# Performance work log

Measured on AMD Instinct MI355X. Metric: run time of the kernel, lower is better.

Reference implementation:

```python
import jax, jax.numpy as jnp
import numpy as np
import math

L, B, S, D, H, DI, V = 4, 2, 1024, 768, 12, 3072, 512
DK = D // H

def gelu_tanh(x):
    c = math.sqrt(2.0 / math.pi)
    return 0.5 * x * (1.0 + jnp.tanh(c * (x + 0.044715 * x ** 3)))

def layer_norm(x, g, b, eps=1e-5):
    mu = jnp.mean(x, axis=-1, keepdims=True)
    var = jnp.var(x, axis=-1, keepdims=True)
    return (x - mu) * jax.lax.rsqrt(var + eps) * g + b

def setup_inputs() -> dict:
    key = jax.random.key(0)
    ks = jax.random.split(key, 12)
    w = 0.02  # init scale
    return {
        "x": jax.random.randint(ks[0], (B, S), 0, V),
        "embed": jax.random.normal(ks[1], (V, D), jnp.float32) * w,
        "pos_emb": jax.random.normal(ks[2], (S, D), jnp.float32) * w,
        "ln1_g": jnp.ones((L, D), jnp.float32),
        "ln1_b": jnp.zeros((L, D), jnp.float32),
        "wq": jax.random.normal(ks[3], (L, D, D), jnp.float32) * w,
        "bq": jnp.zeros((L, D), jnp.float32),
        "wk": jax.random.normal(ks[4], (L, D, D), jnp.float32) * w,
        "bk": jnp.zeros((L, D), jnp.float32),
        "wv": jax.random.normal(ks[5], (L, D, D), jnp.float32) * w,
        "bv": jnp.zeros((L, D), jnp.float32),
        "wo": jax.random.normal(ks[6], (L, D, D), jnp.float32) * w,
        "bo": jnp.zeros((L, D), jnp.float32),
        "ln2_g": jnp.ones((L, D), jnp.float32),
        "ln2_b": jnp.zeros((L, D), jnp.float32),
        "w_in": jax.random.normal(ks[7], (L, D, DI), jnp.float32) * w,
        "b_in": jnp.zeros((L, DI), jnp.float32),
        "w_out": jax.random.normal(ks[8], (L, DI, D), jnp.float32) * w,
        "b_out": jnp.zeros((L, D), jnp.float32),
        "lnf_g": jnp.ones((D,), jnp.float32),
        "lnf_b": jnp.zeros((D,), jnp.float32),
        "out_w": jax.random.normal(ks[9], (D, V), jnp.float32) * w,
    }

def reference(x, embed, pos_emb, ln1_g, ln1_b, wq, bq, wk, bk, wv, bv, wo, bo,
              ln2_g, ln2_b, w_in, b_in, w_out, b_out, lnf_g, lnf_b, out_w):
    s = x.shape[1]
    h = embed[x] + pos_emb[None, :s]                       # [B,S,D]
    causal = jnp.tril(jnp.ones((s, s), bool))              # True = keep
    scale = 1.0 / math.sqrt(DK)
    for l in range(L):
        a = layer_norm(h, ln1_g[l], ln1_b[l])
        q = (a @ wq[l] + bq[l]).reshape(-1, s, H, DK)
        k = (a @ wk[l] + bk[l]).reshape(-1, s, H, DK)
        v = (a @ wv[l] + bv[l]).reshape(-1, s, H, DK)
        scores = jnp.einsum('bqhd,bkhd->bhqk', q, k) * scale
        scores = jnp.where(causal, scores, -jnp.inf)
        attn = jax.nn.softmax(scores, axis=-1)
        o = jnp.einsum('bhqk,bkhd->bqhd', attn, v).reshape(-1, s, D)
        h = h + o @ wo[l] + bo[l]
        f = layer_norm(h, ln2_g[l], ln2_b[l])
        h = h + gelu_tanh(f @ w_in[l] + b_in[l]) @ w_out[l] + b_out[l]
    h = layer_norm(h, lnf_g, lnf_b)
    return h @ out_w                                       # [B,S,V] logits
```

## Files before the change

kernel.cpp:

```cpp
#include <hip/hip_runtime.h>
#include <hip/hip_bf16.h>


#define TKN    2048
#define DMODEL 768
#define SEQ    1024
#define NH     12
#define DHEAD  64
#define DFF    3072
#define NL     4
#define NVOCAB 512
#define NQKV   2304

typedef unsigned short u16;
typedef __attribute__((ext_vector_type(4))) float f32x4;
typedef __attribute__((ext_vector_type(8))) short short8;
typedef __attribute__((ext_vector_type(4))) unsigned short us4;

__device__ __forceinline__ u16 f2bf(float f) {
  unsigned u = __builtin_bit_cast(unsigned, f);
  u += 0x7fffu + ((u >> 16) & 1u);
  return (u16)(u >> 16);
}

__device__ __forceinline__ short8 mk8(us4 lo, us4 hi) {
  short8 r;
  r[0] = (short)lo[0]; r[1] = (short)lo[1]; r[2] = (short)lo[2]; r[3] = (short)lo[3];
  r[4] = (short)hi[0]; r[5] = (short)hi[1]; r[6] = (short)hi[2]; r[7] = (short)hi[3];
  return r;
}

__device__ __forceinline__ void gload16(const u16* g, u16* l) {
  __builtin_amdgcn_global_load_lds(
      (const __attribute__((address_space(1))) unsigned int*)g,
      (__attribute__((address_space(3))) unsigned int*)l, 16, 0, 0);
}

__global__ __launch_bounds__(256) void k_embed(const int* __restrict__ x,
                                               const float* __restrict__ emb,
                                               const float* __restrict__ pos,
                                               float* __restrict__ h) {
  int t = blockIdx.x;
  int s = t & (SEQ - 1);
  int id = x[t];
  int d = threadIdx.x;
#pragma unroll
  for (int j = 0; j < 3; ++j, d += 256)
    h[t * DMODEL + d] = emb[id * DMODEL + d] + pos[s * DMODEL + d];
}

__global__ __launch_bounds__(256) void k_ln(const float* __restrict__ h,
                                            const float* __restrict__ gam,
                                            const float* __restrict__ bet,
                                            u16* __restrict__ out) {
  __shared__ float sbuf[8];
  int row = blockIdx.x, tid = threadIdx.x;
  const float* hr = h + (size_t)row * DMODEL;
  float x0 = hr[tid], x1 = hr[tid + 256], x2 = hr[tid + 512];
  float s = x0 + x1 + x2;
#pragma unroll
  for (int off = 32; off > 0; off >>= 1) s += __shfl_down(s, off);
  if ((tid & 63) == 0) sbuf[tid >> 6] = s;
  __syncthreads();
  float mu = (sbuf[0] + sbuf[1] + sbuf[2] + sbuf[3]) * (1.0f / DMODEL);
  float d0 = x0 - mu, d1 = x1 - mu, d2 = x2 - mu;
  float v = d0 * d0 + d1 * d1 + d2 * d2;
#pragma unroll
  for (int off = 32; off > 0; off >>= 1) v += __shfl_down(v, off);
  if ((tid & 63) == 0) sbuf[4 + (tid >> 6)] = v;
  __syncthreads();
  float var = (sbuf[4] + sbuf[5] + sbuf[6] + sbuf[7]) * (1.0f / DMODEL);
  float rstd = rsqrtf(var + 1e-5f);
  size_t o = (size_t)row * DMODEL;
  out[o + tid]       = f2bf(d0 * rstd * gam[tid]       + bet[tid]);
  out[o + tid + 256] = f2bf(d1 * rstd * gam[tid + 256] + bet[tid + 256]);
  out[o + tid + 512] = f2bf(d2 * rstd * gam[tid + 512] + bet[tid + 512]);
}

__device__ __forceinline__ void cvt_tile(const float* __restrict__ src, int ldS,
                                         int k0, int n0src,
                                         u16* __restrict__ dst, int ldD, int n0dst,
                                         int tid, u16 (*tl)[72]) {
  int kr = tid >> 2, nj = (tid & 3) << 4;
  const float* sp = src + (size_t)(k0 + kr) * ldS + n0src + nj;
  float4 a0 = ((const float4*)sp)[0];
  float4 a1 = ((const float4*)sp)[1];
  float4 a2 = ((const float4*)sp)[2];
  float4 a3 = ((const float4*)sp)[3];
  u16* tr = &tl[kr][nj];
  tr[0]=f2bf(a0.x); tr[1]=f2bf(a0.y); tr[2]=f2bf(a0.z); tr[3]=f2bf(a0.w);
  tr[4]=f2bf(a1.x); tr[5]=f2bf(a1.y); tr[6]=f2bf(a1.z); tr[7]=f2bf(a1.w);
  tr[8]=f2bf(a2.x); tr[9]=f2bf(a2.y); tr[10]=f2bf(a2.z); tr[11]=f2bf(a2.w);
  tr[12]=f2bf(a3.x); tr[13]=f2bf(a3.y); tr[14]=f2bf(a3.z); tr[15]=f2bf(a3.w);
  __syncthreads();
  int nr = tid >> 2, kj = (tid & 3) << 4;
  us4 o[4];
#pragma unroll
  for (int c = 0; c < 4; ++c)
#pragma unroll
    for (int i = 0; i < 4; ++i) o[c][i] = tl[kj + c * 4 + i][nr];
  u16* dp = dst + (size_t)(n0dst + nr) * ldD + k0 + kj;
  ((us4*)dp)[0] = o[0]; ((us4*)dp)[1] = o[1];
  ((us4*)dp)[2] = o[2]; ((us4*)dp)[3] = o[3];
}

__global__ __launch_bounds__(256) void k_cvtL(const float* __restrict__ wq,
                                              const float* __restrict__ wk,
                                              const float* __restrict__ wv,
                                              const float* __restrict__ wo,
                                              const float* __restrict__ win,
                                              const float* __restrict__ wout,
                                              u16* __restrict__ wqkvT,
                                              u16* __restrict__ woT,
                                              u16* __restrict__ winT,
                                              u16* __restrict__ woutT) {
  __shared__ u16 tl[64][72];
  int t = blockIdx.x, tid = threadIdx.x;
  if (t < 432) {
    int kt = t % 12, ntile = t / 12;
    int gn0 = ntile * 64, sel = gn0 / DMODEL;
    const float* src = sel == 0 ? wq : sel == 1 ? wk : wv;
    cvt_tile(src, DMODEL, kt * 64, gn0 - sel * DMODEL, wqkvT, DMODEL, gn0, tid, tl);
  } else if (t < 576) {
    int t2 = t - 432, kt = t2 % 12, nt = t2 / 12;
    cvt_tile(wo, DMODEL, kt * 64, nt * 64, woT, DMODEL, nt * 64, tid, tl);
  } else if (t < 1152) {
    int t3 = t - 576, kt = t3 % 12, nt = t3 / 12;
    cvt_tile(win, DFF, kt * 64, nt * 64, winT, DMODEL, nt * 64, tid, tl);
  } else {
    int t4 = t - 1152, kt = t4 % 48, nt = t4 / 48;
    cvt_tile(wout, DMODEL, kt * 64, nt * 64, woutT, DFF, nt * 64, tid, tl);
  }
}

__global__ __launch_bounds__(256) void k_cvtT(const float* __restrict__ src,
                                              u16* __restrict__ dst,
                                              int K, int N) {
  __shared__ u16 tl[64][72];
  cvt_tile(src, N, blockIdx.x * 64, blockIdx.y * 64, dst, K, blockIdx.y * 64,
           threadIdx.x, tl);
}

__global__ __launch_bounds__(256) void k_packb(const float* __restrict__ bq,
                                               const float* __restrict__ bk,
                                               const float* __restrict__ bv,
                                               float* __restrict__ dst) {
  int i = blockIdx.x * 256 + threadIdx.x;
  if (i < NL * NQKV) {
    int l = i / NQKV, j = i - l * NQKV;
    float v = j < DMODEL ? bq[l * DMODEL + j]
            : j < 2 * DMODEL ? bk[l * DMODEL + j - DMODEL]
            : bv[l * DMODEL + j - 2 * DMODEL];
    dst[i] = v;
  }
}

template <int EP, int BM, int BN>
__global__ __launch_bounds__(256) void k_mm(const u16* __restrict__ A,
                                            const u16* __restrict__ BT,
                                            const float* __restrict__ bias,
                                            void* __restrict__ outp,
                                            int N, int K) {
  constexpr int MI = BM / 32;
  constexpr int NJ = BN / 32;
  __shared__ __align__(16) u16 As[2][BM * 64];
  __shared__ __align__(16) u16 Bs[2][BN * 64];
  const int nbx = gridDim.x;
  int lin = blockIdx.y * nbx + blockIdx.x;
  const int chunk = (nbx * gridDim.y) >> 3;
  lin = (lin & 7) * chunk + (lin >> 3);
  const int bn = (lin % nbx) * BN, bm = (lin / nbx) * BM;

  const int tid = threadIdx.x, lane = tid & 63, wid = tid >> 6;
  const int g = lane >> 4, fl = lane & 15;
  const int wm = wid >> 1, wn = wid & 1;

  const int srow = wid * 8 + (lane >> 3);
  const int scol = ((lane & 7) ^ (lane >> 3)) << 3;
  const u16* ag = A + (size_t)(bm + srow) * K + scol;
  const u16* bg = BT + (size_t)(bn + srow) * K + scol;

  f32x4 acc[MI][NJ] = {};
  const int sw = (fl & 7) << 4;

  auto stage = [&](int buf, int kk) {
#pragma unroll
    for (int is = 0; is < MI; ++is)
      gload16(ag + kk + (size_t)is * 32 * K, &As[buf][wid * 512 + is * 2048]);
#pragma unroll
    for (int is = 0; is < NJ; ++is)
      gload16(bg + kk + (size_t)is * 32 * K, &Bs[buf][wid * 512 + is * 2048]);
  };

  const int ks = K / gridDim.z;
  const int kb0 = blockIdx.z * ks;
  const int nk = ks >> 6;
  stage(0, kb0);
  __syncthreads();
  int cur = 0;
  for (int kt = 0; kt < nk; ++kt) {
    if (kt + 1 < nk) stage(cur ^ 1, kb0 + ((kt + 1) << 6));
#pragma unroll
    for (int k0 = 0; k0 < 64; k0 += 32) {
      const int bo = (k0 + 4 * g) * 2;
      short8 af[MI], bf[NJ];
#pragma unroll
      for (int i = 0; i < MI; ++i) {
        const char* base = (const char*)&As[cur][(wm * (BM / 2) + i * 16 + fl) * 64];
        af[i] = mk8(*(const us4*)(base + (bo ^ sw)),
                    *(const us4*)(base + ((bo + 32) ^ sw)));
      }
#pragma unroll
      for (int j = 0; j < NJ; ++j) {
        const char* base = (const char*)&Bs[cur][(wn * (BN / 2) + j * 16 + fl) * 64];
        bf[j] = mk8(*(const us4*)(base + (bo ^ sw)),
                    *(const us4*)(base + ((bo + 32) ^ sw)));
      }
#pragma unroll
      for (int i = 0; i < MI; ++i)
#pragma unroll
        for (int j = 0; j < NJ; ++j)
          acc[i][j] = __builtin_amdgcn_mfma_f32_16x16x32_bf16(af[i], bf[j], acc[i][j], 0, 0, 0);
    }
    __syncthreads();
    cur ^= 1;
  }

  const int row0 = bm + wm * (BM / 2) + 4 * g;
  const int col0 = bn + wn * (BN / 2) + fl;
#pragma unroll
  for (int j = 0; j < NJ; ++j) {
    int col = col0 + j * 16;
    float bv = (EP == 3) ? 0.0f : bias[col];
    if (EP == 1 && blockIdx.z != 0) bv = 0.0f;
#pragma unroll
    for (int i = 0; i < MI; ++i) {
#pragma unroll
      for (int r = 0; r < 4; ++r) {
        int row = row0 + i * 16 + r;
        float val = acc[i][j][r] + bv;
        size_t idx = (size_t)row * N + col;
        if (EP == 0) {
          ((u16*)outp)[idx] = f2bf(val);
        } else if (EP == 1) {
          atomicAdd(&((float*)outp)[idx], val);
        } else if (EP == 2) {
          float t = 0.7978845608028654f * (val + 0.044715f * val * val * val);
          ((u16*)outp)[idx] = f2bf(0.5f * val * (1.0f + tanhf(t)));
        } else {
          ((float*)outp)[idx] = val;
        }
      }
    }
  }
}

__global__ __launch_bounds__(256) void k_attn(const u16* __restrict__ qkv,
                                              float* __restrict__ pO,
                                              float* __restrict__ pML) {
  __shared__ u16 Vt[2][DHEAD * 68];
  int lin = blockIdx.y * gridDim.x + blockIdx.x;
  const int chunk = (gridDim.x * gridDim.y) >> 3;
  lin = (lin & 7) * chunk + (lin >> 3);
  const int qb = lin % gridDim.x;
  const int bh = lin / gridDim.x;
  const int sp = blockIdx.z;
  const int b = bh / NH, hh = bh % NH;
  const int tid = threadIdx.x, lane = tid & 63, w = tid >> 6;
  const int g = lane >> 4, fl = lane & 15;
  const int qrow = qb * 64 + w * 16 + fl;
  const u16* qp = qkv + (size_t)(b * SEQ + qrow) * NQKV + hh * DHEAD;

  short8 qf[2];
#pragma unroll
  for (int hf = 0; hf < 2; ++hf) {
    us4 lo = *(const us4*)(qp + hf * 32 + 4 * g);
    us4 hi = *(const us4*)(qp + hf * 32 + 16 + 4 * g);
    qf[hf] = mk8(lo, hi);
  }

  float m = -1e30f, lsum = 0.0f;
  f32x4 oacc[4] = {};
  const int qmaxw = qb * 64 + w * 16 + 15;
  const int vr = tid >> 2, vd = (tid & 3) << 4;
  const u16* vbase = qkv + (size_t)(b * SEQ + vr) * NQKV + 2 * DMODEL + hh * DHEAD + vd;
  const u16* kbase0 = qkv + (size_t)(b * SEQ) * NQKV + DMODEL + hh * DHEAD;

  const int nt = qb + 1;
  const int t_lo = (sp * nt) >> 1, t_hi = ((sp + 1) * nt) >> 1;

  if (t_lo < t_hi) {
    {
      const u16* vp = vbase + (size_t)t_lo * 64 * NQKV;
      us4 vv[4];
#pragma unroll
      for (int qi = 0; qi < 4; ++qi) vv[qi] = *(const us4*)(vp + qi * 4);
#pragma unroll
      for (int qi = 0; qi < 4; ++qi)
#pragma unroll
        for (int i = 0; i < 4; ++i) Vt[0][(vd + qi * 4 + i) * 68 + vr] = vv[qi][i];
    }
    __syncthreads();
    int cur = 0;
    for (int t64 = t_lo; t64 < t_hi; ++t64) {
      const u16* kb64 = kbase0 + (size_t)t64 * 64 * NQKV;
      us4 kv[4][4];
#pragma unroll
      for (int q4 = 0; q4 < 4; ++q4) {
        const u16* kp = kb64 + (size_t)(q4 * 16 + fl) * NQKV;
#pragma unroll
        for (int j = 0; j < 4; ++j) kv[q4][j] = *(const us4*)(kp + j * 16 + 4 * g);
      }
      const bool pf = (t64 + 1 < t_hi);
      us4 vvn[4];
      if (pf) {
        const u16* vp = vbase + (size_t)(t64 + 1) * 64 * NQKV;
#pragma unroll
        for (int qi = 0; qi < 4; ++qi) vvn[qi] = *(const us4*)(vp + qi * 4);
      }

#pragma unroll
      for (int i32 = 0; i32 < 2; ++i32) {
        int kb = t64 * 64 + i32 * 32;
        if (kb <= qmaxw) {
          f32x4 sfr[2];
#pragma unroll
          for (int sub = 0; sub < 2; ++sub) {
            int q4 = i32 * 2 + sub;
            short8 kf0 = mk8(kv[q4][0], kv[q4][1]);
            short8 kf1 = mk8(kv[q4][2], kv[q4][3]);
            f32x4 s = {};
            s = __builtin_amdgcn_mfma_f32_16x16x32_bf16(kf0, qf[0], s, 0, 0, 0);
            s = __builtin_amdgcn_mfma_f32_16x16x32_bf16(kf1, qf[1], s, 0, 0, 0);
            sfr[sub] = s;
          }
          float sc[8];
#pragma unroll
          for (int sub = 0; sub < 2; ++sub)
#pragma unroll
            for (int r = 0; r < 4; ++r) {
              int key = kb + sub * 16 + 4 * g + r;
              float sv = sfr[sub][r] * 0.125f;
              sc[sub * 4 + r] = (key <= qrow) ? sv : -1e30f;
            }
          float pmax = sc[0];
#pragma unroll
          for (int e = 1; e < 8; ++e) pmax = fmaxf(pmax, sc[e]);
          pmax = fmaxf(pmax, __shfl_xor(pmax, 16));
          pmax = fmaxf(pmax, __shfl_xor(pmax, 32));
          if (__all(pmax <= m + 8.0f)) {
            float p[8], ps = 0.0f;
#pragma unroll
            for (int e = 0; e < 8; ++e) { p[e] = __expf(sc[e] - m); ps += p[e]; }
            ps += __shfl_xor(ps, 16);
            ps += __shfl_xor(ps, 32);
            lsum += ps;
            short8 pfr;
#pragma unroll
            for (int e = 0; e < 8; ++e) pfr[e] = (short)f2bf(p[e]);
#pragma unroll
            for (int nb = 0; nb < 4; ++nb) {
              const u16* vtp = &Vt[cur][(nb * 16 + fl) * 68 + i32 * 32 + 4 * g];
              short8 vf = mk8(*(const us4*)vtp, *(const us4*)(vtp + 16));
              oacc[nb] = __builtin_amdgcn_mfma_f32_16x16x32_bf16(pfr, vf, oacc[nb], 0, 0, 0);
            }
          } else {
            float mnew = fmaxf(m, pmax);
            float corr = __expf(m - mnew);
            float p[8], ps = 0.0f;
#pragma unroll
            for (int e = 0; e < 8; ++e) { p[e] = __expf(sc[e] - mnew); ps += p[e]; }
            ps += __shfl_xor(ps, 16);
            ps += __shfl_xor(ps, 32);
            lsum = lsum * corr + ps;
            m = mnew;
            float cr[4];
#pragma unroll
            for (int r = 0; r < 4; ++r) cr[r] = __shfl(corr, 4 * g + r);
#pragma unroll
            for (int nb = 0; nb < 4; ++nb)
#pragma unroll
              for (int r = 0; r < 4; ++r) oacc[nb][r] *= cr[r];
            short8 pfr;
#pragma unroll
            for (int e = 0; e < 8; ++e) pfr[e] = (short)f2bf(p[e]);
#pragma unroll
            for (int nb = 0; nb < 4; ++nb) {
              const u16* vtp = &Vt[cur][(nb * 16 + fl) * 68 + i32 * 32 + 4 * g];
              short8 vf = mk8(*(const us4*)vtp, *(const us4*)(vtp + 16));
              oacc[nb] = __builtin_amdgcn_mfma_f32_16x16x32_bf16(pfr, vf, oacc[nb], 0, 0, 0);
            }
          }
        }
      }
      if (pf) {
        __syncthreads();
#pragma unroll
        for (int qi = 0; qi < 4; ++qi)
#pragma unroll
          for (int i = 0; i < 4; ++i) Vt[cur ^ 1][(vd + qi * 4 + i) * 68 + vr] = vvn[qi][i];
        __syncthreads();
        cur ^= 1;
      }
    }
  }

  const size_t part = ((size_t)bh * 16 + qb) * 2 + sp;
  float* ob = pO + part * 4096;
  float* ml = pML + part * 128;
#pragma unroll
  for (int nb = 0; nb < 4; ++nb)
#pragma unroll
    for (int r = 0; r < 4; ++r)
      ob[(w * 16 + 4 * g + r) * 64 + nb * 16 + fl] = oacc[nb][r];
  if (g == 0) {
    ml[w * 16 + fl] = m;
    ml[64 + w * 16 + fl] = lsum;
  }
}

__global__ __launch_bounds__(256) void k_ared(const float* __restrict__ pO,
                                              const float* __restrict__ pML,
                                              u16* __restrict__ O) {
  __shared__ float w0s[64], w1s[64], iLs[64];
  const int qb = blockIdx.x, bh = blockIdx.y;
  const int b = bh / NH, hh = bh % NH;
  const int tid = threadIdx.x;
  const size_t p0 = ((size_t)bh * 16 + qb) * 2;
  if (tid < 64) {
    float m0 = pML[p0 * 128 + tid], l0 = pML[p0 * 128 + 64 + tid];
    float m1 = pML[(p0 + 1) * 128 + tid], l1 = pML[(p0 + 1) * 128 + 64 + tid];
    float M = fmaxf(m0, m1);
    float w0 = __expf(m0 - M), w1 = __expf(m1 - M);
    w0s[tid] = w0; w1s[tid] = w1;
    iLs[tid] = 1.0f / (l0 * w0 + l1 * w1);
  }
  __syncthreads();
  const float* O0 = pO + p0 * 4096;
  const float* O1 = pO + (p0 + 1) * 4096;
  for (int i = tid; i < 4096; i += 256) {
    int row = i >> 6, d = i & 63;
    float v = (O0[i] * w0s[row] + O1[i] * w1s[row]) * iLs[row];
    O[(size_t)(b * SEQ + qb * 64 + row) * DMODEL + hh * DHEAD + d] = f2bf(v);
  }
}

extern "C" void kernel_launch(void* const* d_in, const int* in_sizes, int n_in,
                              void* d_out, int out_size, void* d_ws, size_t ws_size,
                              hipStream_t stream) {
  const int*   x    = (const int*)d_in[0];
  const float* emb  = (const float*)d_in[1];
  const float* pos  = (const float*)d_in[2];
  const float* ln1g = (const float*)d_in[3];
  const float* ln1b = (const float*)d_in[4];
  const float* wq   = (const float*)d_in[5];
  const float* bq   = (const float*)d_in[6];
  const float* wk   = (const float*)d_in[7];
  const float* bk   = (const float*)d_in[8];
  const float* wv   = (const float*)d_in[9];
  const float* bv   = (const float*)d_in[10];
  const float* wo   = (const float*)d_in[11];
  const float* bo   = (const float*)d_in[12];
  const float* ln2g = (const float*)d_in[13];
  const float* ln2b = (const float*)d_in[14];
  const float* win  = (const float*)d_in[15];
  const float* bin  = (const float*)d_in[16];
  const float* wout = (const float*)d_in[17];
  const float* bout = (const float*)d_in[18];
  const float* lnfg = (const float*)d_in[19];
  const float* lnfb = (const float*)d_in[20];
  const float* outw = (const float*)d_in[21];

  char* w8 = (char*)d_ws;
  float* h    = (float*)(w8);
  u16* abuf   = (u16*)(w8 + 6291456);
  u16* qkv    = (u16*)(w8 + 9437184);
  u16* obuf   = (u16*)(w8 + 18874368);
  u16* ffbuf  = (u16*)(w8 + 9437184);
  u16* wqkvT  = (u16*)(w8 + 22020096);
  u16* woT    = (u16*)(w8 + 25559040);
  u16* winT   = (u16*)(w8 + 26738688);
  u16* woutT  = (u16*)(w8 + 31457280);
  u16* outwT  = (u16*)(w8 + 36175872);
  float* bqkv = (float*)(w8 + 36962304);
  float* pO   = (float*)(w8 + 36999168);
  float* pML  = (float*)(w8 + 49582080);

  k_embed<<<TKN, 256, 0, stream>>>(x, emb, pos, h);
  k_packb<<<36, 256, 0, stream>>>(bq, bk, bv, bqkv);
  k_cvtT<<<dim3(12, 8), 256, 0, stream>>>(outw, outwT, DMODEL, NVOCAB);

  for (int l = 0; l < NL; ++l) {
    k_cvtL<<<1728, 256, 0, stream>>>(
        wq + (size_t)l * DMODEL * DMODEL, wk + (size_t)l * DMODEL * DMODEL,
        wv + (size_t)l * DMODEL * DMODEL, wo + (size_t)l * DMODEL * DMODEL,
        win + (size_t)l * DMODEL * DFF, wout + (size_t)l * DFF * DMODEL,
        wqkvT, woT, winT, woutT);

    k_ln<<<TKN, 256, 0, stream>>>(h, ln1g + l * DMODEL, ln1b + l * DMODEL, abuf);
    k_mm<0, 128, 64><<<dim3(NQKV / 64, TKN / 128, 1), 256, 0, stream>>>(
        abuf, wqkvT, bqkv + l * NQKV, qkv, NQKV, DMODEL);
    k_attn<<<dim3(SEQ / 64, 2 * NH, 2), 256, 0, stream>>>(qkv, pO, pML);
    k_ared<<<dim3(SEQ / 64, 2 * NH), 256, 0, stream>>>(pO, pML, obuf);
    k_mm<1, 128, 64><<<dim3(DMODEL / 64, TKN / 128, 2), 256, 0, stream>>>(
        obuf, woT, bo + l * DMODEL, h, DMODEL, DMODEL);
    k_ln<<<TKN, 256, 0, stream>>>(h, ln2g + l * DMODEL, ln2b + l * DMODEL, abuf);
    k_mm<2, 128, 64><<<dim3(DFF / 64, TKN / 128, 1), 256, 0, stream>>>(
        abuf, winT, bin + l * DFF, ffbuf, DFF, DMODEL);
    k_mm<1, 128, 64><<<dim3(DMODEL / 64, TKN / 128, 4), 256, 0, stream>>>(
        ffbuf, woutT, bout + l * DMODEL, h, DMODEL, DFF);
  }

  k_ln<<<TKN, 256, 0, stream>>>(h, lnfg, lnfb, abuf);
  k_mm<3, 64, 64><<<dim3(NVOCAB / 64, TKN / 64, 1), 256, 0, stream>>>(
      abuf, outwT, nullptr, d_out, NVOCAB, DMODEL);
}
```

Measured before the change: 709.8 us.

## Rebalance causal attention split-K per query block and store bf16 partials

Attention now runs on a flat 960-block grid where the number of key splits grows with the query block index (1 to 4), so each block does a similar amount of causal work. The inner loop handles all 64 keys per tile at once and applies the causal mask only on the diagonal tile. The 1/8 softmax scale is folded into Q by lowering the bf16 exponent, and `s_setprio` is raised around the MFMA sections. Partial outputs are written as bf16 to cut reduction traffic, with the statistics buffer moved into the idle LN scratch region. This costs some precision in the partial sums and adds a variable-split reduction loop.

```diff
diff --git a/kernel.cpp b/kernel.cpp
--- a/kernel.cpp
+++ b/kernel.cpp
@@ -21,6 +21,16 @@
   unsigned u = __builtin_bit_cast(unsigned, f);
   u += 0x7fffu + ((u >> 16) & 1u);
   return (u16)(u >> 16);
+}
+
+__device__ __forceinline__ float bf2f(u16 u) {
+  unsigned v = ((unsigned)u) << 16;
+  return __builtin_bit_cast(float, v);
+}
+
+__device__ __forceinline__ u16 bf_eighth(u16 u) {
+  int e = (u >> 7) & 0xFF;
+  return e >= 3 ? (u16)(u - (3 << 7)) : (u16)(u & 0x8000);
 }
 
 __device__ __forceinline__ short8 mk8(us4 lo, us4 hi) {
@@ -256,15 +266,21 @@
 }
 
 __global__ __launch_bounds__(256) void k_attn(const u16* __restrict__ qkv,
-                                              float* __restrict__ pO,
+                                              u16* __restrict__ pO,
                                               float* __restrict__ pML) {
   __shared__ u16 Vt[2][DHEAD * 68];
-  int lin = blockIdx.y * gridDim.x + blockIdx.x;
-  const int chunk = (gridDim.x * gridDim.y) >> 3;
-  lin = (lin & 7) * chunk + (lin >> 3);
-  const int qb = lin % gridDim.x;
-  const int bh = lin / gridDim.x;
-  const int sp = blockIdx.z;
+  int bid = blockIdx.x;
+  int lin = (bid & 7) * 120 + (bid >> 3);
+  const int bh = lin / 40;
+  const int idx = lin - bh * 40;
+  int qb, sp;
+  if (idx < 4)       { qb = idx;                     sp = 0; }
+  else if (idx < 12) { qb = 4 + ((idx - 4) >> 1);    sp = (idx - 4) & 1; }
+  else if (idx < 24) { int t = idx - 12; qb = 8 + t / 3;  sp = t - (t / 3) * 3; }
+  else               { int t = idx - 24; qb = 12 + (t >> 2); sp = t & 3; }
+  const int nsp = 1 + (qb >> 2), nt = qb + 1;
+  const int t_lo = sp * nt / nsp, t_hi = (sp + 1) * nt / nsp;
+
   const int b = bh / NH, hh = bh % NH;
   const int tid = threadIdx.x, lane = tid & 63, w = tid >> 6;
   const int g = lane >> 4, fl = lane & 15;
@@ -276,172 +292,176 @@
   for (int hf = 0; hf < 2; ++hf) {
     us4 lo = *(const us4*)(qp + hf * 32 + 4 * g);
     us4 hi = *(const us4*)(qp + hf * 32 + 16 + 4 * g);
+#pragma unroll
+    for (int i = 0; i < 4; ++i) { lo[i] = bf_eighth(lo[i]); hi[i] = bf_eighth(hi[i]); }
     qf[hf] = mk8(lo, hi);
   }
 
   float m = -1e30f, lsum = 0.0f;
   f32x4 oacc[4] = {};
-  const int qmaxw = qb * 64 + w * 16 + 15;
   const int vr = tid >> 2, vd = (tid & 3) << 4;
   const u16* vbase = qkv + (size_t)(b * SEQ + vr) * NQKV + 2 * DMODEL + hh * DHEAD + vd;
   const u16* kbase0 = qkv + (size_t)(b * SEQ) * NQKV + DMODEL + hh * DHEAD;
 
-  const int nt = qb + 1;
-  const int t_lo = (sp * nt) >> 1, t_hi = ((sp + 1) * nt) >> 1;
-
-  if (t_lo < t_hi) {
-    {
-      const u16* vp = vbase + (size_t)t_lo * 64 * NQKV;
-      us4 vv[4];
-#pragma unroll
-      for (int qi = 0; qi < 4; ++qi) vv[qi] = *(const us4*)(vp + qi * 4);
+  {
+    const u16* vp = vbase + (size_t)t_lo * 64 * NQKV;
+    us4 vv[4];
+#pragma unroll
+    for (int qi = 0; qi < 4; ++qi) vv[qi] = *(const us4*)(vp + qi * 4);
+#pragma unroll
+    for (int qi = 0; qi < 4; ++qi)
+#pragma unroll
+      for (int i = 0; i < 4; ++i) Vt[0][(vd + qi * 4 + i) * 68 + vr] = vv[qi][i];
+  }
+  __syncthreads();
+  int cur = 0;
+
+  for (int t64 = t_lo; t64 < t_hi; ++t64) {
+    const u16* kb64 = kbase0 + (size_t)t64 * 64 * NQKV;
+    us4 kv[4][4];
+#pragma unroll
+    for (int q4 = 0; q4 < 4; ++q4) {
+      const u16* kp = kb64 + (size_t)(q4 * 16 + fl) * NQKV;
+#pragma unroll
+      for (int j = 0; j < 4; ++j) kv[q4][j] = *(const us4*)(kp + j * 16 + 4 * g);
+    }
+    const bool pf = (t64 + 1 < t_hi);
+    us4 vvn[4];
+    if (pf) {
+      const u16* vp = vbase + (size_t)(t64 + 1) * 64 * NQKV;
+#pragma unroll
+      for (int qi = 0; qi < 4; ++qi) vvn[qi] = *(const us4*)(vp + qi * 4);
+    }
+
+    f32x4 sfr[4];
+    __builtin_amdgcn_s_setprio(1);
+#pragma unroll
+    for (int sub = 0; sub < 4; ++sub) {
+      short8 kf0 = mk8(kv[sub][0], kv[sub][1]);
+      short8 kf1 = mk8(kv[sub][2], kv[sub][3]);
+      f32x4 s = {};
+      s = __builtin_amdgcn_mfma_f32_16x16x32_bf16(kf0, qf[0], s, 0, 0, 0);
+      s = __builtin_amdgcn_mfma_f32_16x16x32_bf16(kf1, qf[1], s, 0, 0, 0);
+      sfr[sub] = s;
+    }
+    __builtin_amdgcn_s_setprio(0);
+
+    float sc[16];
+    if (t64 == qb) {
+#pragma unroll
+      for (int sub = 0; sub < 4; ++sub)
+#pragma unroll
+        for (int r = 0; r < 4; ++r) {
+          int key = t64 * 64 + sub * 16 + 4 * g + r;
+          sc[sub * 4 + r] = (key <= qrow) ? sfr[sub][r] : -1e30f;
+        }
+    } else {
+#pragma unroll
+      for (int sub = 0; sub < 4; ++sub)
+#pragma unroll
+        for (int r = 0; r < 4; ++r) sc[sub * 4 + r] = sfr[sub][r];
+    }
+    float pmax = sc[0];
+#pragma unroll
+    for (int e = 1; e < 16; ++e) pmax = fmaxf(pmax, sc[e]);
+    pmax = fmaxf(pmax, __shfl_xor(pmax, 16));
+    pmax = fmaxf(pmax, __shfl_xor(pmax, 32));
+
+    float p[16];
+    if (__all(pmax <= m + 8.0f)) {
+      float ps = 0.0f;
+#pragma unroll
+      for (int e = 0; e < 16; ++e) { p[e] = __expf(sc[e] - m); ps += p[e]; }
+      ps += __shfl_xor(ps, 16);
+      ps += __shfl_xor(ps, 32);
+      lsum += ps;
+    } else {
+      float mnew = fmaxf(m, pmax);
+      float corr = __expf(m - mnew);
+      float ps = 0.0f;
+#pragma unroll
+      for (int e = 0; e < 16; ++e) { p[e] = __expf(sc[e] - mnew); ps += p[e]; }
+      ps += __shfl_xor(ps, 16);
+      ps += __shfl_xor(ps, 32);
+      lsum = lsum * corr + ps;
+      m = mnew;
+      float cr[4];
+#pragma unroll
+      for (int r = 0; r < 4; ++r) cr[r] = __shfl(corr, 4 * g + r);
+#pragma unroll
+      for (int nb = 0; nb < 4; ++nb)
+#pragma unroll
+        for (int r = 0; r < 4; ++r) oacc[nb][r] *= cr[r];
+    }
+
+    short8 pf0, pf1;
+#pragma unroll
+    for (int e = 0; e < 8; ++e) { pf0[e] = (short)f2bf(p[e]); pf1[e] = (short)f2bf(p[8 + e]); }
+
+    __builtin_amdgcn_s_setprio(1);
+#pragma unroll
+    for (int nb = 0; nb < 4; ++nb) {
+      const u16* vtp = &Vt[cur][(nb * 16 + fl) * 68 + 4 * g];
+      short8 vf0 = mk8(*(const us4*)vtp, *(const us4*)(vtp + 16));
+      short8 vf1 = mk8(*(const us4*)(vtp + 32), *(const us4*)(vtp + 48));
+      oacc[nb] = __builtin_amdgcn_mfma_f32_16x16x32_bf16(pf0, vf0, oacc[nb], 0, 0, 0);
+      oacc[nb] = __builtin_amdgcn_mfma_f32_16x16x32_bf16(pf1, vf1, oacc[nb], 0, 0, 0);
+    }
+    __builtin_amdgcn_s_setprio(0);
+
+    if (pf) {
+      __syncthreads();
 #pragma unroll
       for (int qi = 0; qi < 4; ++qi)
 #pragma unroll
-        for (int i = 0; i < 4; ++i) Vt[0][(vd + qi * 4 + i) * 68 + vr] = vv[qi][i];
-    }
-    __syncthreads();
-    int cur = 0;
-    for (int t64 = t_lo; t64 < t_hi; ++t64) {
-      const u16* kb64 = kbase0 + (size_t)t64 * 64 * NQKV;
-      us4 kv[4][4];
-#pragma unroll
-      for (int q4 = 0; q4 < 4; ++q4) {
-        const u16* kp = kb64 + (size_t)(q4 * 16 + fl) * NQKV;
-#pragma unroll
-        for (int j = 0; j < 4; ++j) kv[q4][j] = *(const us4*)(kp + j * 16 + 4 * g);
-      }
-      const bool pf = (t64 + 1 < t_hi);
-      us4 vvn[4];
-      if (pf) {
-        const u16* vp = vbase + (size_t)(t64 + 1) * 64 * NQKV;
-#pragma unroll
-        for (int qi = 0; qi < 4; ++qi) vvn[qi] = *(const us4*)(vp + qi * 4);
-      }
-
-#pragma unroll
-      for (int i32 = 0; i32 < 2; ++i32) {
-        int kb = t64 * 64 + i32 * 32;
-        if (kb <= qmaxw) {
-          f32x4 sfr[2];
-#pragma unroll
-          for (int sub = 0; sub < 2; ++sub) {
-            int q4 = i32 * 2 + sub;
-            short8 kf0 = mk8(kv[q4][0], kv[q4][1]);
-            short8 kf1 = mk8(kv[q4][2], kv[q4][3]);
-            f32x4 s = {};
-            s = __builtin_amdgcn_mfma_f32_16x16x32_bf16(kf0, qf[0], s, 0, 0, 0);
-            s = __builtin_amdgcn_mfma_f32_16x16x32_bf16(kf1, qf[1], s, 0, 0, 0);
-            sfr[sub] = s;
-          }
-          float sc[8];
-#pragma unroll
-          for (int sub = 0; sub < 2; ++sub)
-#pragma unroll
-            for (int r = 0; r < 4; ++r) {
-              int key = kb + sub * 16 + 4 * g + r;
-              float sv = sfr[sub][r] * 0.125f;
-              sc[sub * 4 + r] = (key <= qrow) ? sv : -1e30f;
-            }
-          float pmax = sc[0];
-#pragma unroll
-          for (int e = 1; e < 8; ++e) pmax = fmaxf(pmax, sc[e]);
-          pmax = fmaxf(pmax, __shfl_xor(pmax, 16));
-          pmax = fmaxf(pmax, __shfl_xor(pmax, 32));
-          if (__all(pmax <= m + 8.0f)) {
-            float p[8], ps = 0.0f;
-#pragma unroll
-            for (int e = 0; e < 8; ++e) { p[e] = __expf(sc[e] - m); ps += p[e]; }
-            ps += __shfl_xor(ps, 16);
-            ps += __shfl_xor(ps, 32);
-            lsum += ps;
-            short8 pfr;
-#pragma unroll
-            for (int e = 0; e < 8; ++e) pfr[e] = (short)f2bf(p[e]);
-#pragma unroll
-            for (int nb = 0; nb < 4; ++nb) {
-              const u16* vtp = &Vt[cur][(nb * 16 + fl) * 68 + i32 * 32 + 4 * g];
-              short8 vf = mk8(*(const us4*)vtp, *(const us4*)(vtp + 16));
-              oacc[nb] = __builtin_amdgcn_mfma_f32_16x16x32_bf16(pfr, vf, oacc[nb], 0, 0, 0);
-            }
-          } else {
-            float mnew = fmaxf(m, pmax);
-            float corr = __expf(m - mnew);
-            float p[8], ps = 0.0f;
-#pragma unroll
-            for (int e = 0; e < 8; ++e) { p[e] = __expf(sc[e] - mnew); ps += p[e]; }
-            ps += __shfl_xor(ps, 16);
-            ps += __shfl_xor(ps, 32);
-            lsum = lsum * corr + ps;
-            m = mnew;
-            float cr[4];
-#pragma unroll
-            for (int r = 0; r < 4; ++r) cr[r] = __shfl(corr, 4 * g + r);
-#pragma unroll
-            for (int nb = 0; nb < 4; ++nb)
-#pragma unroll
-              for (int r = 0; r < 4; ++r) oacc[nb][r] *= cr[r];
-            short8 pfr;
-#pragma unroll
-            for (int e = 0; e < 8; ++e) pfr[e] = (short)f2bf(p[e]);
-#pragma unroll
-            for (int nb = 0; nb < 4; ++nb) {
-              const u16* vtp = &Vt[cur][(nb * 16 + fl) * 68 + i32 * 32 + 4 * g];
-              short8 vf = mk8(*(const us4*)vtp, *(const us4*)(vtp + 16));
-              oacc[nb] = __builtin_amdgcn_mfma_f32_16x16x32_bf16(pfr, vf, oacc[nb], 0, 0, 0);
-            }
-          }
-        }
-      }
-      if (pf) {
-        __syncthreads();
-#pragma unroll
-        for (int qi = 0; qi < 4; ++qi)
-#pragma unroll
-          for (int i = 0; i < 4; ++i) Vt[cur ^ 1][(vd + qi * 4 + i) * 68 + vr] = vvn[qi][i];
-        __syncthreads();
-        cur ^= 1;
-      }
-    }
-  }
-
-  const size_t part = ((size_t)bh * 16 + qb) * 2 + sp;
-  float* ob = pO + part * 4096;
+        for (int i = 0; i < 4; ++i) Vt[cur ^ 1][(vd + qi * 4 + i) * 68 + vr] = vvn[qi][i];
+      __syncthreads();
+      cur ^= 1;
+    }
+  }
+
+  const size_t part = ((size_t)bh * 16 + qb) * 4 + sp;
+  u16* ob = pO + part * 4096;
   float* ml = pML + part * 128;
 #pragma unroll
   for (int nb = 0; nb < 4; ++nb)
 #pragma unroll
     for (int r = 0; r < 4; ++r)
-      ob[(w * 16 + 4 * g + r) * 64 + nb * 16 + fl] = oacc[nb][r];
+      ob[(w * 16 + 4 * g + r) * 64 + nb * 16 + fl] = f2bf(oacc[nb][r]);
   if (g == 0) {
     ml[w * 16 + fl] = m;
     ml[64 + w * 16 + fl] = lsum;
   }
 }
 
-__global__ __launch_bounds__(256) void k_ared(const float* __restrict__ pO,
+__global__ __launch_bounds__(256) void k_ared(const u16* __restrict__ pO,
                                               const float* __restrict__ pML,
                                               u16* __restrict__ O) {
-  __shared__ float w0s[64], w1s[64], iLs[64];
+  __shared__ float wgt[4][64];
+  __shared__ float iLs[64];
   const int qb = blockIdx.x, bh = blockIdx.y;
+  const int nsp = 1 + (qb >> 2);
   const int b = bh / NH, hh = bh % NH;
   const int tid = threadIdx.x;
-  const size_t p0 = ((size_t)bh * 16 + qb) * 2;
+  const size_t p0 = ((size_t)bh * 16 + qb) * 4;
   if (tid < 64) {
-    float m0 = pML[p0 * 128 + tid], l0 = pML[p0 * 128 + 64 + tid];
-    float m1 = pML[(p0 + 1) * 128 + tid], l1 = pML[(p0 + 1) * 128 + 64 + tid];
-    float M = fmaxf(m0, m1);
-    float w0 = __expf(m0 - M), w1 = __expf(m1 - M);
-    w0s[tid] = w0; w1s[tid] = w1;
-    iLs[tid] = 1.0f / (l0 * w0 + l1 * w1);
+    float M = -1e30f;
+    for (int s = 0; s < nsp; ++s) M = fmaxf(M, pML[(p0 + s) * 128 + tid]);
+    float L = 0.0f;
+    for (int s = 0; s < nsp; ++s) {
+      float wv = __expf(pML[(p0 + s) * 128 + tid] - M);
+      wgt[s][tid] = wv;
+      L += pML[(p0 + s) * 128 + 64 + tid] * wv;
+    }
+    iLs[tid] = 1.0f / L;
   }
   __syncthreads();
-  const float* O0 = pO + p0 * 4096;
-  const float* O1 = pO + (p0 + 1) * 4096;
   for (int i = tid; i < 4096; i += 256) {
     int row = i >> 6, d = i & 63;
-    float v = (O0[i] * w0s[row] + O1[i] * w1s[row]) * iLs[row];
-    O[(size_t)(b * SEQ + qb * 64 + row) * DMODEL + hh * DHEAD + d] = f2bf(v);
+    float acc = 0.0f;
+    for (int s = 0; s < nsp; ++s)
+      acc += bf2f(pO[(p0 + s) * 4096 + i]) * wgt[s][row];
+    O[(size_t)(b * SEQ + qb * 64 + row) * DMODEL + hh * DHEAD + d] = f2bf(acc * iLs[row]);
   }
 }
 
@@ -483,8 +503,10 @@
   u16* woutT  = (u16*)(w8 + 31457280);
   u16* outwT  = (u16*)(w8 + 36175872);
   float* bqkv = (float*)(w8 + 36962304);
-  float* pO   = (float*)(w8 + 36999168);
-  float* pML  = (float*)(w8 + 49582080);
+  u16* pO     = (u16*)(w8 + 36999168);
+  float* pML  = (float*)(w8 + 6291456 + 0);
+
+  pML = (float*)(w8 + 6291456);
 
   k_embed<<<TKN, 256, 0, stream>>>(x, emb, pos, h);
   k_packb<<<36, 256, 0, stream>>>(bq, bk, bv, bqkv);
@@ -500,7 +522,7 @@
     k_ln<<<TKN, 256, 0, stream>>>(h, ln1g + l * DMODEL, ln1b + l * DMODEL, abuf);
     k_mm<0, 128, 64><<<dim3(NQKV / 64, TKN / 128, 1), 256, 0, stream>>>(
         abuf, wqkvT, bqkv + l * NQKV, qkv, NQKV, DMODEL);
-    k_attn<<<dim3(SEQ / 64, 2 * NH, 2), 256, 0, stream>>>(qkv, pO, pML);
+    k_attn<<<960, 256, 0, stream>>>(qkv, pO, pML);
     k_ared<<<dim3(SEQ / 64, 2 * NH), 256, 0, stream>>>(pO, pML, obuf);
     k_mm<1, 128, 64><<<dim3(DMODEL / 64, TKN / 128, 2), 256, 0, stream>>>(
         obuf, woT, bo + l * DMODEL, h, DMODEL, DMODEL);
```

Measured after the change: 713.3 us. No clear change (+0.5%).
